# Kernel optimization log

Hardware: AMD Instinct MI355X
Metric: run time of the kernel (lower is better)

## Reference

```python
import jax, jax.numpy as jnp
import numpy as np

N_HEAD = 16
D_MODEL = 1024
D_HEAD = 64
SCALE = 1.0 / D_HEAD ** 0.5
LN_EPS = 1e-5


def layer_norm(x, g, b):
    mu = jnp.mean(x, axis=-1, keepdims=True)
    var = jnp.mean(jnp.square(x - mu), axis=-1, keepdims=True)
    return (x - mu) * jax.lax.rsqrt(var + LN_EPS) * g + b


def setup_inputs() -> dict:
    key = jax.random.key(0)
    ks = jax.random.split(key, 6)
    T, B = 2048, 4
    h = jax.random.normal(ks[0], (T, B, D_MODEL), dtype=jnp.float32)
    # key-padding mask, shape (klen, bsz); True = masked
    attn_mask = jax.random.randint(ks[1], (T, B), 0, 2).astype(jnp.bool_)
    s = 1.0 / np.sqrt(D_MODEL)
    wq = jax.random.uniform(ks[2], (N_HEAD * D_HEAD, D_MODEL), minval=-s, maxval=s, dtype=jnp.float32)
    wkv = jax.random.uniform(ks[3], (2 * N_HEAD * D_HEAD, D_MODEL), minval=-s, maxval=s, dtype=jnp.float32)
    wo = jax.random.uniform(ks[4], (D_MODEL, N_HEAD * D_HEAD), minval=-s, maxval=s, dtype=jnp.float32)
    ln_g = jnp.ones((D_MODEL,), jnp.float32)
    ln_b = jnp.zeros((D_MODEL,), jnp.float32)
    return {"h": h, "attn_mask": attn_mask, "wq": wq, "wkv": wkv,
            "wo": wo, "ln_g": ln_g, "ln_b": ln_b}


def reference(h, attn_mask, wq, wkv, wo, ln_g, ln_b):
    T, B, _ = h.shape
    c = h  # mems is None
    head_q = (h @ wq.T).reshape(T, B, N_HEAD, D_HEAD)
    kv = c @ wkv.T
    head_k, head_v = jnp.split(kv, 2, axis=-1)
    head_k = head_k.reshape(T, B, N_HEAD, D_HEAD)
    head_v = head_v.reshape(T, B, N_HEAD, D_HEAD)

    # scores: [qlen, klen, bsz, n_head]
    attn_score = jnp.einsum('ibnd,jbnd->ijbn', head_q, head_k) * SCALE
    attn_score = jnp.where(attn_mask[None, :, :, None], -jnp.inf, attn_score)
    attn_prob = jax.nn.softmax(attn_score, axis=1)

    attn_vec = jnp.einsum('ijbn,jbnd->ibnd', attn_prob, head_v)
    attn_vec = attn_vec.reshape(T, B, N_HEAD * D_HEAD)
    attn_out = attn_vec @ wo.T
    # post-lnorm residual (pre_lnorm=False); gate='plus' path unused here
    return layer_norm(h + attn_out, ln_g, ln_b)
```

## Files before the change

kernel.cpp:

```cpp
#include <hip/hip_runtime.h>

#define T_LEN 2048
#define BSZ 4
#define NHEAD 16
#define DHEAD 64
#define DMODEL 1024
#define SCALE 0.125f
#define L2E_SCALE (0.125f * 1.44269504f)

typedef __bf16 bf16x8 __attribute__((ext_vector_type(8)));
typedef float f32x4 __attribute__((ext_vector_type(4)));

__device__ __forceinline__ float bf2f(unsigned short u) {
  union { unsigned int i; float f; } v; v.i = ((unsigned int)u) << 16; return v.f;
}
__device__ __forceinline__ unsigned short f2bf(float f) {
  union { float f; unsigned int i; } v; v.f = f;
  unsigned int r = v.i + 0x7fffu + ((v.i >> 16) & 1u);
  return (unsigned short)(r >> 16);
}

typedef __attribute__((address_space(1))) void* gptr_t;
typedef __attribute__((address_space(3))) void* lptr_t;

__device__ __forceinline__ void load_lds16(const void* g, void* l) {
  __builtin_amdgcn_global_load_lds((gptr_t)g, (lptr_t)l, 16, 0, 0);
}

__device__ __forceinline__ int swz16(int row, int g) {
  return row * 64 + ((g ^ (row & 7)) << 3);
}

__global__ __launch_bounds__(256) void cvt_prep(const float* __restrict__ h,
                                                const float* __restrict__ wq,
                                                const float* __restrict__ wkv,
                                                const float* __restrict__ wo,
                                                const unsigned char* __restrict__ mask,
                                                unsigned short* __restrict__ h_bf,
                                                unsigned short* __restrict__ wq_bf,
                                                unsigned short* __restrict__ wkv_bf,
                                                unsigned short* __restrict__ wo_bf,
                                                int* __restrict__ pos,
                                                int* __restrict__ nkeys) {
  const int tid = threadIdx.x;
  if (blockIdx.x < 12288) {
    const size_t E4 = (size_t)T_LEN * BSZ * DMODEL / 4;
    const size_t W4 = (size_t)NHEAD * DHEAD * DMODEL / 4;
    const size_t g = (size_t)blockIdx.x * 256 + tid;
    const float* src; unsigned short* dst; size_t off;
    if (g < E4)                { src = h;   dst = h_bf;   off = g; }
    else if (g < E4 + W4)      { src = wq;  dst = wq_bf;  off = g - E4; }
    else if (g < E4 + 3 * W4)  { src = wkv; dst = wkv_bf; off = g - E4 - W4; }
    else                       { src = wo;  dst = wo_bf;  off = g - E4 - 3 * W4; }
    const float4 v = *(const float4*)(src + off * 4);
    ushort4 o;
    o.x = f2bf(v.x); o.y = f2bf(v.y); o.z = f2bf(v.z); o.w = f2bf(v.w);
    *(ushort4*)(dst + off * 4) = o;
    return;
  }
  __shared__ int s_any;
  if (tid == 0) s_any = 0;
  __syncthreads();
  int acc = 0;
  for (int i = tid; i < T_LEN * BSZ; i += 256)
    if ((i & 3) != 0 && mask[i] != 0) acc = 1;
  if (acc) atomicOr(&s_any, 1);
  __syncthreads();
  const int mmode = s_any ? 0 : 1;
  const int wv = tid >> 6, lane = tid & 63;
  const int b = wv;
  int run = 0;
  for (int j0 = 0; j0 < T_LEN; j0 += 64) {
    const int j = j0 + lane;
    const int mval = mmode ? ((const int*)mask)[(size_t)j * BSZ + b]
                           : (int)mask[(size_t)j * BSZ + b];
    const int keep = (mval == 0) ? 1 : 0;
    int x = keep;
#pragma unroll
    for (int off = 1; off < 64; off <<= 1) {
      const int y = __shfl_up(x, off, 64);
      if (lane >= off) x += y;
    }
    pos[b * T_LEN + j] = keep ? (run + x - keep) : -1;
    run += __shfl(x, 63, 64);
  }
  if (lane == 0) nkeys[b] = run;
}

#define GEMM64_DBUF(Aptr, Bptr)                                                        \
  const int tid  = threadIdx.x;                                                        \
  const int lane = tid & 63;                                                           \
  const int wv   = tid >> 6;                                                           \
  const int wr = (wv >> 1) * 64;                                                       \
  const int wc = (wv & 1) * 64;                                                        \
  const int mi   = lane & 15;                                                          \
  const int quad = lane >> 4;                                                          \
  f32x4 acc[4][4] = {};                                                                \
  int rowc[4], colc[4];                                                                \
  _Pragma("unroll")                                                                    \
  for (int c = 0; c < 4; c++) {                                                        \
    const int s = c * 256 + tid;                                                       \
    rowc[c] = s >> 3;                                                                  \
    colc[c] = ((s & 7) ^ (rowc[c] & 7)) * 8;                                           \
  }                                                                                    \
  const int swz = mi & 7;                                                              \
  _Pragma("unroll")                                                                    \
  for (int c = 0; c < 4; c++) {                                                        \
    load_lds16(Aptr + (size_t)rowc[c] * DMODEL + colc[c], As + c * 2048 + wv * 512);   \
    load_lds16(Bptr + (size_t)rowc[c] * DMODEL + colc[c], Bs + c * 2048 + wv * 512);   \
  }                                                                                    \
  for (int k0 = 0; k0 < DMODEL; k0 += 64) {                                            \
    const int cur = (k0 >> 6) & 1;                                                     \
    const unsigned short* Asr = As + cur * 8192;                                       \
    const unsigned short* Bsr = Bs + cur * 8192;                                       \
    unsigned short* Asw = As + (1 - cur) * 8192;                                       \
    unsigned short* Bsw = Bs + (1 - cur) * 8192;                                       \
    __syncthreads();                                                                   \
    if (k0 + 64 < DMODEL) {                                                            \
      _Pragma("unroll")                                                                \
      for (int c = 0; c < 4; c++) {                                                    \
        load_lds16(Aptr + (size_t)rowc[c] * DMODEL + k0 + 64 + colc[c], Asw + c * 2048 + wv * 512); \
        load_lds16(Bptr + (size_t)rowc[c] * DMODEL + k0 + 64 + colc[c], Bsw + c * 2048 + wv * 512); \
      }                                                                                \
    }                                                                                  \
    _Pragma("unroll")                                                                  \
    for (int kq = 0; kq < 2; kq++) {                                                   \
      const int cp = ((kq * 4 + quad) ^ swz) * 8;                                      \
      bf16x8 af[4], bfr[4];                                                            \
      _Pragma("unroll")                                                                \
      for (int rt = 0; rt < 4; rt++)                                                   \
        af[rt] = *(const bf16x8*)(Asr + (wr + rt * 16 + mi) * 64 + cp);                \
      _Pragma("unroll")                                                                \
      for (int ct = 0; ct < 4; ct++)                                                   \
        bfr[ct] = *(const bf16x8*)(Bsr + (wc + ct * 16 + mi) * 64 + cp);               \
      _Pragma("unroll")                                                                \
      for (int rt = 0; rt < 4; rt++)                                                   \
        _Pragma("unroll")                                                              \
        for (int ct = 0; ct < 4; ct++)                                                 \
          acc[rt][ct] = __builtin_amdgcn_mfma_f32_16x16x32_bf16(af[rt], bfr[ct], acc[rt][ct], 0, 0, 0); \
    }                                                                                  \
  }

__global__ __launch_bounds__(256) void gemm_qkv(const unsigned short* __restrict__ A,
                                                const unsigned short* __restrict__ Wq,
                                                const unsigned short* __restrict__ Wkv,
                                                const int* __restrict__ pos,
                                                unsigned short* __restrict__ outQ,
                                                unsigned short* __restrict__ outK,
                                                unsigned short* __restrict__ outVt) {
  __shared__ alignas(16) unsigned short As[2 * 128 * 64];
  __shared__ alignas(16) unsigned short Bs[2 * 128 * 64];
  const int m0 = blockIdx.y * 128;
  const int n0 = blockIdx.x * 128;
  const unsigned short* Abase = A + (size_t)m0 * DMODEL;
  const unsigned short* Bbase = (n0 < DMODEL) ? (Wq + (size_t)n0 * DMODEL)
                                              : (Wkv + (size_t)(n0 - DMODEL) * DMODEL);
  GEMM64_DBUF(Abase, Bbase)

  const int region = n0 >> 10;
#pragma unroll
  for (int rt = 0; rt < 4; rt++) {
#pragma unroll
    for (int r = 0; r < 4; r++) {
      const int gm = m0 + wr + rt * 16 + quad * 4 + r;
      const int i = gm >> 2, b = gm & 3;
      int p = i;
      if (region > 0) p = pos[b * T_LEN + i];
      if (region > 0 && p < 0) continue;
#pragma unroll
      for (int ct = 0; ct < 4; ct++) {
        const int gn = n0 + wc + ct * 16 + mi;
        const int gnl = gn & (DMODEL - 1);
        const int hn = gnl >> 6, d = gnl & 63;
        const float v = acc[rt][ct][r];
        if (region == 0)
          outQ[(((size_t)b * NHEAD + hn) * T_LEN + i) * DHEAD + d] = f2bf(v * L2E_SCALE);
        else if (region == 1)
          outK[(((size_t)b * NHEAD + hn) * T_LEN + p) * DHEAD + d] = f2bf(v);
        else
          outVt[(((size_t)b * NHEAD + hn) * DHEAD + d) * T_LEN + p] = f2bf(v);
      }
    }
  }
}

__global__ __launch_bounds__(256) void gemm_out(const unsigned short* __restrict__ A,
                                                const unsigned short* __restrict__ Bw,
                                                unsigned short* __restrict__ outB) {
  __shared__ alignas(16) unsigned short As[2 * 128 * 64];
  __shared__ alignas(16) unsigned short Bs[2 * 128 * 64];
  const int m0 = blockIdx.y * 128;
  const int n0 = blockIdx.x * 128;
  const unsigned short* Abase = A  + (size_t)m0 * DMODEL;
  const unsigned short* Bbase = Bw + (size_t)n0 * DMODEL;
  GEMM64_DBUF(Abase, Bbase)

#pragma unroll
  for (int rt = 0; rt < 4; rt++)
#pragma unroll
    for (int ct = 0; ct < 4; ct++)
#pragma unroll
      for (int r = 0; r < 4; r++) {
        const int gm = m0 + wr + rt * 16 + quad * 4 + r;
        const int gn = n0 + wc + ct * 16 + mi;
        outB[(size_t)gm * DMODEL + gn] = f2bf(acc[rt][ct][r]);
      }
}

template<bool TAIL>
__device__ __forceinline__ void attn_chunk(int j0, int nk, int mi, int quad,
    const unsigned short* Ks, const unsigned short* Vts, unsigned short* PsW,
    const bf16x8 (&qb)[2][2], f32x4 (&oc)[2][4], float (&rs)[2]) {
  f32x4 sc[2][4] = {};
#pragma unroll
  for (int ct = 0; ct < 4; ct++) {
    const bf16x8 kf0 = *(const bf16x8*)(Ks + swz16(ct * 16 + mi, quad));
    const bf16x8 kf1 = *(const bf16x8*)(Ks + swz16(ct * 16 + mi, 4 + quad));
#pragma unroll
    for (int g = 0; g < 2; g++) {
      sc[g][ct] = __builtin_amdgcn_mfma_f32_16x16x32_bf16(kf0, qb[g][0], sc[g][ct], 0, 0, 0);
      sc[g][ct] = __builtin_amdgcn_mfma_f32_16x16x32_bf16(kf1, qb[g][1], sc[g][ct], 0, 0, 0);
    }
  }
#pragma unroll
  for (int g = 0; g < 2; g++)
#pragma unroll
    for (int ct = 0; ct < 4; ct++) {
#pragma unroll
      for (int r = 0; r < 4; r++) {
        float p = __builtin_amdgcn_exp2f(sc[g][ct][r]);
        if (TAIL && (j0 + ct * 16 + quad * 4 + r >= nk)) p = 0.f;
        rs[g] += p;
        sc[g][ct][r] = p;
      }
      union { float f; unsigned u; } c0, c1, c2, c3;
      c0.f = sc[g][ct][0]; c1.f = sc[g][ct][1]; c2.f = sc[g][ct][2]; c3.f = sc[g][ct][3];
      const unsigned pk0 = (c0.u >> 16) | (c1.u & 0xFFFF0000u);
      const unsigned pk1 = (c2.u >> 16) | (c3.u & 0xFFFF0000u);
      const int prow = g * 16 + mi;
      *(uint2*)(PsW + prow * 64 + (((2 * ct + (quad >> 1)) ^ (prow & 7)) << 3)
                + (quad & 1) * 4) = make_uint2(pk0, pk1);
    }
  bf16x8 pa0[2], pa1[2];
#pragma unroll
  for (int g = 0; g < 2; g++) {
    pa0[g] = *(const bf16x8*)(PsW + swz16(g * 16 + mi, quad));
    pa1[g] = *(const bf16x8*)(PsW + swz16(g * 16 + mi, 4 + quad));
  }
#pragma unroll
  for (int ct = 0; ct < 4; ct++) {
    const bf16x8 vf0 = *(const bf16x8*)(Vts + swz16(ct * 16 + mi, quad));
    const bf16x8 vf1 = *(const bf16x8*)(Vts + swz16(ct * 16 + mi, 4 + quad));
#pragma unroll
    for (int g = 0; g < 2; g++) {
      oc[g][ct] = __builtin_amdgcn_mfma_f32_16x16x32_bf16(pa0[g], vf0, oc[g][ct], 0, 0, 0);
      oc[g][ct] = __builtin_amdgcn_mfma_f32_16x16x32_bf16(pa1[g], vf1, oc[g][ct], 0, 0, 0);
    }
  }
}

__global__ __launch_bounds__(256, 4) void attn_mfma(const unsigned short* __restrict__ Qg,
                                                    const unsigned short* __restrict__ Kg,
                                                    const unsigned short* __restrict__ Vtg,
                                                    const int* __restrict__ nkeys,
                                                    unsigned short* __restrict__ av) {
  __shared__ alignas(16) unsigned short smem[16640];
  unsigned short* Ks  = smem;
  unsigned short* Vts = smem + 4096;
  unsigned short* Qs  = smem + 8192;
  float* Ls = (float*)(smem + 16384);

  const int tid  = threadIdx.x;
  const int lane = tid & 63;
  const int wv   = tid >> 6;
  const int mi   = lane & 15;
  const int quad = lane >> 4;
  const int i0 = blockIdx.x * 128;
  const int b  = blockIdx.y;
  const int n  = blockIdx.z;
  const size_t base = ((size_t)b * NHEAD + n) * T_LEN * DHEAD;
  const int nk = nkeys[b];

  for (int it = tid; it < 1024; it += 256) {
    const int r = it >> 3, g = it & 7;
    *(uint4*)(Qs + swz16(r, g)) = *(const uint4*)(Qg + base + (size_t)(i0 + r) * DHEAD + g * 8);
  }
  __syncthreads();
  bf16x8 qb[2][2];
#pragma unroll
  for (int g = 0; g < 2; g++) {
    qb[g][0] = *(const bf16x8*)(Qs + swz16(wv * 32 + g * 16 + mi, quad));
    qb[g][1] = *(const bf16x8*)(Qs + swz16(wv * 32 + g * 16 + mi, 4 + quad));
  }

  f32x4 oc[2][4] = {};
  float rs[2] = {0.f, 0.f};
  unsigned short* PsW = Qs + wv * 2048;

  const int nmain = nk & ~63;
  for (int j0 = 0; j0 < nmain; j0 += 64) {
    for (int it = tid; it < 512; it += 256) {
      const int r = it >> 3, g = it & 7;
      *(uint4*)(Ks  + swz16(r, g)) = *(const uint4*)(Kg  + base + (size_t)(j0 + r) * DHEAD + g * 8);
      *(uint4*)(Vts + swz16(r, g)) = *(const uint4*)(Vtg + base + (size_t)r * T_LEN + j0 + g * 8);
    }
    __syncthreads();
    attn_chunk<false>(j0, nk, mi, quad, Ks, Vts, PsW, qb, oc, rs);
    __syncthreads();
  }
  if (nmain < nk) {
    for (int it = tid; it < 512; it += 256) {
      const int r = it >> 3, g = it & 7;
      *(uint4*)(Ks  + swz16(r, g)) = *(const uint4*)(Kg  + base + (size_t)(nmain + r) * DHEAD + g * 8);
      *(uint4*)(Vts + swz16(r, g)) = *(const uint4*)(Vtg + base + (size_t)r * T_LEN + nmain + g * 8);
    }
    __syncthreads();
    attn_chunk<true>(nmain, nk, mi, quad, Ks, Vts, PsW, qb, oc, rs);
  }

#pragma unroll
  for (int g = 0; g < 2; g++) {
    float t = rs[g];
    t += __shfl_xor(t, 16, 64);
    t += __shfl_xor(t, 32, 64);
    rs[g] = t;
  }
  if (quad == 0) { Ls[wv * 32 + mi] = rs[0]; Ls[wv * 32 + 16 + mi] = rs[1]; }
  __syncthreads();
  float linv[2][4];
#pragma unroll
  for (int g = 0; g < 2; g++)
#pragma unroll
    for (int r = 0; r < 4; r++) {
      const float l = Ls[wv * 32 + g * 16 + quad * 4 + r];
      linv[g][r] = (l > 0.f) ? (1.f / l) : 0.f;
    }
#pragma unroll
  for (int g = 0; g < 2; g++)
#pragma unroll
    for (int ct = 0; ct < 4; ct++)
#pragma unroll
      for (int r = 0; r < 4; r++) {
        const int q = i0 + wv * 32 + g * 16 + quad * 4 + r;
        const int d = ct * 16 + mi;
        av[((size_t)q * BSZ + b) * DMODEL + n * DHEAD + d] = f2bf(oc[g][ct][r] * linv[g][r]);
      }
}

__global__ __launch_bounds__(256) void ln_kernel(const float* __restrict__ h,
                                                 const unsigned short* __restrict__ ao,
                                                 const float* __restrict__ g,
                                                 const float* __restrict__ bb,
                                                 float* __restrict__ out) {
  __shared__ float red[16];
  const int row = blockIdx.x;
  const int tid = threadIdx.x;
  const size_t base = (size_t)row * DMODEL;
  const int c = tid * 4;
  const float4 hv = *(const float4*)(h + base + c);
  const ushort4 a4 = *(const ushort4*)(ao + base + c);
  float x[4] = { hv.x + bf2f(a4.x), hv.y + bf2f(a4.y), hv.z + bf2f(a4.z), hv.w + bf2f(a4.w) };
  float s = 0.f, sq = 0.f;
#pragma unroll
  for (int k = 0; k < 4; k++) { s += x[k]; sq += x[k] * x[k]; }
#pragma unroll
  for (int off = 32; off; off >>= 1) { s += __shfl_xor(s, off, 64); sq += __shfl_xor(sq, off, 64); }
  const int wv = tid >> 6, lane = tid & 63;
  if (lane == 0) { red[wv] = s; red[8 + wv] = sq; }
  __syncthreads();
  if (tid == 0) {
    float ts = 0.f, tq = 0.f;
    for (int w = 0; w < 4; w++) { ts += red[w]; tq += red[8 + w]; }
    red[4] = ts; red[12] = tq;
  }
  __syncthreads();
  const float mu  = red[4] * (1.f / DMODEL);
  const float var = red[12] * (1.f / DMODEL) - mu * mu;
  const float inv = rsqrtf(var + 1e-5f);
  const float4 gv = *(const float4*)(g + c);
  const float4 bv = *(const float4*)(bb + c);
  float4 o;
  o.x = (x[0] - mu) * inv * gv.x + bv.x;
  o.y = (x[1] - mu) * inv * gv.y + bv.y;
  o.z = (x[2] - mu) * inv * gv.z + bv.z;
  o.w = (x[3] - mu) * inv * gv.w + bv.w;
  *(float4*)(out + base + c) = o;
}

extern "C" void kernel_launch(void* const* d_in, const int* in_sizes, int n_in,
                              void* d_out, int out_size, void* d_ws, size_t ws_size,
                              hipStream_t stream) {
  (void)in_sizes; (void)n_in; (void)out_size; (void)ws_size;
  const float* h           = (const float*)d_in[0];
  const unsigned char* msk = (const unsigned char*)d_in[1];
  const float* wq          = (const float*)d_in[2];
  const float* wkv         = (const float*)d_in[3];
  const float* wo          = (const float*)d_in[4];
  const float* lng         = (const float*)d_in[5];
  const float* lnb         = (const float*)d_in[6];
  float* out = (float*)d_out;

  const size_t E  = (size_t)T_LEN * BSZ * DMODEL;
  const size_t WQ = (size_t)NHEAD * DHEAD * DMODEL;
  char* ws = (char*)d_ws;
  int* nkeys            = (int*)ws;                       ws += 16;
  int* pos              = (int*)ws;                       ws += (size_t)BSZ * T_LEN * 4;
  unsigned short* h_bf  = (unsigned short*)ws;            ws += E * 2;
  unsigned short* wq_bf = (unsigned short*)ws;            ws += WQ * 2;
  unsigned short* wkv_bf= (unsigned short*)ws;            ws += 2 * WQ * 2;
  unsigned short* wo_bf = (unsigned short*)ws;            ws += WQ * 2;
  unsigned short* Qb    = (unsigned short*)ws;            ws += E * 2;
  unsigned short* Kb    = (unsigned short*)ws;            ws += E * 2;
  unsigned short* Vtb   = (unsigned short*)ws;            ws += E * 2;
  unsigned short* AV    = (unsigned short*)ws;            ws += E * 2;
  unsigned short* AO    = (unsigned short*)ws;

  const dim3 blk(256);
  cvt_prep<<<dim3(12289), blk, 0, stream>>>(h, wq, wkv, wo, msk,
                                            h_bf, wq_bf, wkv_bf, wo_bf, pos, nkeys);
  gemm_qkv<<<dim3(3 * DMODEL / 128, T_LEN * BSZ / 128), blk, 0, stream>>>(
      h_bf, wq_bf, wkv_bf, pos, Qb, Kb, Vtb);
  attn_mfma<<<dim3(T_LEN / 128, BSZ, NHEAD), blk, 0, stream>>>(Qb, Kb, Vtb, nkeys, AV);
  gemm_out<<<dim3(DMODEL / 128, T_LEN * BSZ / 128), blk, 0, stream>>>(AV, wo_bf, AO);
  ln_kernel<<<dim3(T_LEN * BSZ), blk, 0, stream>>>(h, AO, lng, lnb, out);
}
```

Baseline: 314.7 us.

## Double-buffer K/V tiles with async LDS loads in attention; one-row-per-wave layernorm

The attention kernel now keeps two K/V buffers in shared memory and issues direct global-to-LDS loads for the next 64-key chunk while computing the current one. This replaces the synchronous load, barrier, compute, barrier sequence and removes one barrier per chunk. It raises shared memory use and lowers the occupancy hint from 4 to 3. Separately, the layernorm kernel processes one row per wavefront, so it needs only shuffle reductions and no block-level barriers.

Result: faster. 308.2 us (-2.0%).

```diff
diff --git a/kernel.cpp b/kernel.cpp
--- a/kernel.cpp
+++ b/kernel.cpp
@@ -259,16 +259,30 @@
   }
 }
 
-__global__ __launch_bounds__(256, 4) void attn_mfma(const unsigned short* __restrict__ Qg,
+__device__ __forceinline__ void stage_kv(const unsigned short* __restrict__ Kg,
+                                         const unsigned short* __restrict__ Vtg,
+                                         size_t base, int j0s, unsigned short* kb,
+                                         int tid, int wv) {
+#pragma unroll
+  for (int u = 0; u < 2; u++) {
+    const int gi = u * 256 + tid;
+    const int r = gi >> 3;
+    const int gs = (gi ^ r) & 7;
+    load_lds16(Kg + base + (size_t)(j0s + r) * DHEAD + gs * 8,
+               kb + u * 2048 + wv * 512);
+    load_lds16(Vtg + base + (size_t)r * T_LEN + j0s + gs * 8,
+               kb + 4096 + u * 2048 + wv * 512);
+  }
+}
+
+__global__ __launch_bounds__(256, 3) void attn_mfma(const unsigned short* __restrict__ Qg,
                                                     const unsigned short* __restrict__ Kg,
                                                     const unsigned short* __restrict__ Vtg,
                                                     const int* __restrict__ nkeys,
                                                     unsigned short* __restrict__ av) {
-  __shared__ alignas(16) unsigned short smem[16640];
-  unsigned short* Ks  = smem;
-  unsigned short* Vts = smem + 4096;
-  unsigned short* Qs  = smem + 8192;
-  float* Ls = (float*)(smem + 16384);
+  __shared__ alignas(16) unsigned short smem[24832];
+  unsigned short* Qs = smem + 16384;
+  float* Ls = (float*)(smem + 24576);
 
   const int tid  = threadIdx.x;
   const int lane = tid & 63;
@@ -280,11 +294,13 @@
   const int n  = blockIdx.z;
   const size_t base = ((size_t)b * NHEAD + n) * T_LEN * DHEAD;
   const int nk = nkeys[b];
+  const int nc = (nk + 63) >> 6;
 
   for (int it = tid; it < 1024; it += 256) {
     const int r = it >> 3, g = it & 7;
     *(uint4*)(Qs + swz16(r, g)) = *(const uint4*)(Qg + base + (size_t)(i0 + r) * DHEAD + g * 8);
   }
+  if (nc > 0) stage_kv(Kg, Vtg, base, 0, smem, tid, wv);
   __syncthreads();
   bf16x8 qb[2][2];
 #pragma unroll
@@ -297,25 +313,15 @@
   float rs[2] = {0.f, 0.f};
   unsigned short* PsW = Qs + wv * 2048;
 
-  const int nmain = nk & ~63;
-  for (int j0 = 0; j0 < nmain; j0 += 64) {
-    for (int it = tid; it < 512; it += 256) {
-      const int r = it >> 3, g = it & 7;
-      *(uint4*)(Ks  + swz16(r, g)) = *(const uint4*)(Kg  + base + (size_t)(j0 + r) * DHEAD + g * 8);
-      *(uint4*)(Vts + swz16(r, g)) = *(const uint4*)(Vtg + base + (size_t)r * T_LEN + j0 + g * 8);
-    }
+  for (int c = 0; c < nc; ++c) {
+    if (c + 1 < nc) stage_kv(Kg, Vtg, base, (c + 1) * 64, smem + ((c + 1) & 1) * 8192, tid, wv);
+    const unsigned short* Kl = smem + (c & 1) * 8192;
+    const unsigned short* Vl = Kl + 4096;
+    if (c == nc - 1 && (nk & 63))
+      attn_chunk<true>(c * 64, nk, mi, quad, Kl, Vl, PsW, qb, oc, rs);
+    else
+      attn_chunk<false>(c * 64, nk, mi, quad, Kl, Vl, PsW, qb, oc, rs);
     __syncthreads();
-    attn_chunk<false>(j0, nk, mi, quad, Ks, Vts, PsW, qb, oc, rs);
-    __syncthreads();
-  }
-  if (nmain < nk) {
-    for (int it = tid; it < 512; it += 256) {
-      const int r = it >> 3, g = it & 7;
-      *(uint4*)(Ks  + swz16(r, g)) = *(const uint4*)(Kg  + base + (size_t)(nmain + r) * DHEAD + g * 8);
-      *(uint4*)(Vts + swz16(r, g)) = *(const uint4*)(Vtg + base + (size_t)r * T_LEN + nmain + g * 8);
-    }
-    __syncthreads();
-    attn_chunk<true>(nmain, nk, mi, quad, Ks, Vts, PsW, qb, oc, rs);
   }
 
 #pragma unroll
@@ -352,39 +358,40 @@
                                                  const float* __restrict__ g,
                                                  const float* __restrict__ bb,
                                                  float* __restrict__ out) {
-  __shared__ float red[16];
-  const int row = blockIdx.x;
-  const int tid = threadIdx.x;
+  const int tid = threadIdx.x, lane = tid & 63, wv = tid >> 6;
+  const int row = blockIdx.x * 4 + wv;
   const size_t base = (size_t)row * DMODEL;
-  const int c = tid * 4;
-  const float4 hv = *(const float4*)(h + base + c);
-  const ushort4 a4 = *(const ushort4*)(ao + base + c);
-  float x[4] = { hv.x + bf2f(a4.x), hv.y + bf2f(a4.y), hv.z + bf2f(a4.z), hv.w + bf2f(a4.w) };
+  float x[16];
   float s = 0.f, sq = 0.f;
 #pragma unroll
-  for (int k = 0; k < 4; k++) { s += x[k]; sq += x[k] * x[k]; }
+  for (int k = 0; k < 4; k++) {
+    const int c = lane * 4 + k * 256;
+    const float4 hv = *(const float4*)(h + base + c);
+    const ushort4 a4 = *(const ushort4*)(ao + base + c);
+    x[k * 4 + 0] = hv.x + bf2f(a4.x);
+    x[k * 4 + 1] = hv.y + bf2f(a4.y);
+    x[k * 4 + 2] = hv.z + bf2f(a4.z);
+    x[k * 4 + 3] = hv.w + bf2f(a4.w);
+#pragma unroll
+    for (int j = 0; j < 4; j++) { s += x[k * 4 + j]; sq += x[k * 4 + j] * x[k * 4 + j]; }
+  }
 #pragma unroll
   for (int off = 32; off; off >>= 1) { s += __shfl_xor(s, off, 64); sq += __shfl_xor(sq, off, 64); }
-  const int wv = tid >> 6, lane = tid & 63;
-  if (lane == 0) { red[wv] = s; red[8 + wv] = sq; }
-  __syncthreads();
-  if (tid == 0) {
-    float ts = 0.f, tq = 0.f;
-    for (int w = 0; w < 4; w++) { ts += red[w]; tq += red[8 + w]; }
-    red[4] = ts; red[12] = tq;
-  }
-  __syncthreads();
-  const float mu  = red[4] * (1.f / DMODEL);
-  const float var = red[12] * (1.f / DMODEL) - mu * mu;
+  const float mu  = s * (1.f / DMODEL);
+  const float var = sq * (1.f / DMODEL) - mu * mu;
   const float inv = rsqrtf(var + 1e-5f);
-  const float4 gv = *(const float4*)(g + c);
-  const float4 bv = *(const float4*)(bb + c);
-  float4 o;
-  o.x = (x[0] - mu) * inv * gv.x + bv.x;
-  o.y = (x[1] - mu) * inv * gv.y + bv.y;
-  o.z = (x[2] - mu) * inv * gv.z + bv.z;
-  o.w = (x[3] - mu) * inv * gv.w + bv.w;
-  *(float4*)(out + base + c) = o;
+#pragma unroll
+  for (int k = 0; k < 4; k++) {
+    const int c = lane * 4 + k * 256;
+    const float4 gv = *(const float4*)(g + c);
+    const float4 bv = *(const float4*)(bb + c);
+    float4 o;
+    o.x = (x[k * 4 + 0] - mu) * inv * gv.x + bv.x;
+    o.y = (x[k * 4 + 1] - mu) * inv * gv.y + bv.y;
+    o.z = (x[k * 4 + 2] - mu) * inv * gv.z + bv.z;
+    o.w = (x[k * 4 + 3] - mu) * inv * gv.w + bv.w;
+    *(float4*)(out + base + c) = o;
+  }
 }
 
 extern "C" void kernel_launch(void* const* d_in, const int* in_sizes, int n_in,
@@ -422,5 +429,5 @@
       h_bf, wq_bf, wkv_bf, pos, Qb, Kb, Vtb);
   attn_mfma<<<dim3(T_LEN / 128, BSZ, NHEAD), blk, 0, stream>>>(Qb, Kb, Vtb, nkeys, AV);
   gemm_out<<<dim3(DMODEL / 128, T_LEN * BSZ / 128), blk, 0, stream>>>(AV, wo_bf, AO);
-  ln_kernel<<<dim3(T_LEN * BSZ), blk, 0, stream>>>(h, AO, lng, lnb, out);
-}
+  ln_kernel<<<dim3(T_LEN * BSZ / 4), blk, 0, stream>>>(h, AO, lng, lnb, out);
+}
```
